# Performance work log

Hardware: AMD Instinct MI355X
Metric: run time of the kernel (lower is better)

## Reference

```python
import jax, jax.numpy as jnp
import numpy as np

H, W = 224, 224
NF, IN_NF, NL = 32, 100, 4


def conv2d(x, w):
    # 3x3 same-padding conv, NCHW / OIHW
    return jax.lax.conv_general_dilated(x, w, (1, 1), [(1, 1), (1, 1)],
                                        dimension_numbers=('NCHW', 'OIHW', 'NCHW'))


def prelu(x, a):
    return jnp.where(x >= 0, x, a[None, :, None, None] * x)


def bilinear_warp(x, flow):
    # backward warp: sample x at (grid + flow), border clamping
    B, C, Hh, Ww = x.shape
    yy, xx = jnp.meshgrid(jnp.arange(Hh, dtype=x.dtype), jnp.arange(Ww, dtype=x.dtype), indexing='ij')
    px = xx[None] + flow[:, 0]  # [B,H,W]
    py = yy[None] + flow[:, 1]
    x0 = jnp.floor(px); y0 = jnp.floor(py)
    wx = (px - x0)[:, None]; wy = (py - y0)[:, None]  # [B,1,H,W]
    cx = lambda v: jnp.clip(v, 0, Ww - 1).astype(jnp.int32)
    cy = lambda v: jnp.clip(v, 0, Hh - 1).astype(jnp.int32)
    x0i, x1i = cx(x0), cx(x0 + 1)
    y0i, y1i = cy(y0), cy(y0 + 1)
    gather = jax.vmap(lambda img, yi, xi: img[:, yi, xi])  # per-batch fancy gather -> [C,H,W]
    I00 = gather(x, y0i, x0i); I01 = gather(x, y0i, x1i)
    I10 = gather(x, y1i, x0i); I11 = gather(x, y1i, x1i)
    return I00 * (1 - wx) * (1 - wy) + I01 * wx * (1 - wy) + I10 * (1 - wx) * wy + I11 * wx * wy


def glblock_forward(feat_0, feat_1, feat_dense, flow, space_mask,
                    w_head, a_head, w_blocks, a_blocks, w_last, b_last, w_mask, b_mask):
    f0w = bilinear_warp(feat_0, flow[:, :2])
    f1w = bilinear_warp(feat_1, flow[:, 2:4])
    x = jnp.concatenate([f0w, f1w, feat_dense, flow], axis=1)  # [1, in_nf, H, W]
    mask_up = jnp.repeat(jnp.repeat(space_mask, 2, axis=2), 2, axis=3)
    # head: conv3x3 (no bias) + PReLU, then spatial masking
    x = prelu(conv2d(x, w_head), a_head) * space_mask
    outs = [x]
    for i in range(w_blocks.shape[0]):
        x = prelu(conv2d(x, w_blocks[i]) * space_mask, a_blocks[i])
        outs.append(x)
    feats = jnp.concatenate(outs, axis=1)  # [1, in_nf*(NL+1), H, W]
    x = jnp.einsum('oi,bihw->bohw', w_last, feats) + b_last[None, :, None, None]  # 1x1 conv
    smn = conv2d(x[:, 4:], w_mask) + b_mask[None, :, None, None]  # [1,2,H,W]
    B, C, Hh, Ww = x.shape
    xu = jax.image.resize(x, (B, C, 2 * Hh, 2 * Ww), 'linear')
    smnu = jax.image.resize(smn, (B, 2, 2 * Hh, 2 * Ww), 'linear')
    flow_out = xu[:, :4]
    feat_t = xu[:, 4:]
    # eval-mode hard routing mask (training uses gumbel-softmax)
    mask_next = (smnu[:, :1] > smnu[:, 1:]).astype(x.dtype) * mask_up
    return flow_out, feat_t, mask_next


def setup_inputs() -> dict:
    key = jax.random.key(0)
    ks = jax.random.split(key, 12)
    r = lambda i, shape, s=1.0: jax.random.normal(ks[i], shape, jnp.float32) * s
    return {
        'feat_0': r(0, (1, NF, H, W)),
        'feat_1': r(1, (1, NF, H, W)),
        'feat_dense': r(2, (1, NF, H, W)),
        'flow': r(3, (1, 4, H, W)),
        'space_mask': jax.random.uniform(ks[4], (1, 1, H, W), jnp.float32),
        'w_head': r(5, (IN_NF, IN_NF, 3, 3), 0.02),
        'a_head': jnp.full((IN_NF,), 0.25, jnp.float32),
        'w_blocks': r(6, (NL, IN_NF, IN_NF, 3, 3), 0.02),
        'a_blocks': jnp.full((NL, IN_NF), 0.25, jnp.float32),
        'w_last': r(7, (4 + NF, IN_NF * (NL + 1)), 0.02),
        'b_last': r(8, (4 + NF,), 0.02),
        'w_mask': r(9, (2, NF, 3, 3), 0.02),
        'b_mask': r(10, (2,), 0.02),
    }


def reference(feat_0, feat_1, feat_dense, flow, space_mask,
              w_head, a_head, w_blocks, a_blocks, w_last, b_last, w_mask, b_mask):
    return glblock_forward(feat_0, feat_1, feat_dense, flow, space_mask,
                           w_head, a_head, w_blocks, a_blocks, w_last, b_last, w_mask, b_mask)
```

## Files before the change

kernel.cpp:

```cpp
#include <hip/hip_runtime.h>
#include <hip/hip_bf16.h>

#define HWs 50176
#define WID 224
#define OHW 200704

typedef __attribute__((ext_vector_type(8))) short s16x8;
typedef __attribute__((ext_vector_type(4))) float f32x4;

static __device__ __forceinline__ unsigned short f2bf(float x) {
  unsigned u = __float_as_uint(x);
  unsigned r = (u + 0x7fffu + ((u >> 16) & 1u)) >> 16;
  return (unsigned short)r;
}
static __device__ __forceinline__ float bf2f(unsigned short b) {
  return __uint_as_float(((unsigned)b) << 16);
}

__global__ void k_wt(const float* __restrict__ w_head, const float* __restrict__ w_blk,
                     unsigned short* __restrict__ bw) {
  int gid = blockIdx.x * 256 + threadIdx.x;
  int frag = gid >> 7, rr = gid & 127;
  int spl = rr >> 6, lane = rr & 63;
  int l = frag / 288, q = frag - l * 288;
  int t = q / 32, q2 = q - t * 32;
  int ck = q2 >> 3, nt = q2 & 7;
  int oc = nt * 16 + (lane & 15);
  int kg = lane >> 4;
  const float* src = (l == 0) ? w_head : (w_blk + (size_t)(l - 1) * 90000);
  s16x8 outv;
  #pragma unroll
  for (int e = 0; e < 8; ++e) {
    int ic = ck * 32 + kg * 8 + e;
    float w = (oc < 100 && ic < 100) ? src[oc * 900 + ic * 9 + t] : 0.f;
    unsigned short h = f2bf(w);
    unsigned short lo = f2bf(w - bf2f(h));
    outv[e] = (short)(spl ? lo : h);
  }
  ((s16x8*)bw)[gid] = outv;
}

__global__ void k_wlT(const float* __restrict__ wlast, float* __restrict__ wlT) {
  int i = blockIdx.x * 256 + threadIdx.x;
  if (i < 18000) {
    int il = i / 36, o = i - il * 36;
    wlT[i] = wlast[o * 500 + il];
  }
}

__global__ void k_binit(const float* __restrict__ blast, float* __restrict__ xlast) {
  int p = blockIdx.x * 256 + threadIdx.x;
  xlast[(size_t)blockIdx.y * HWs + p] = blast[blockIdx.y];
}

__global__ void k_warp(const float* __restrict__ f0, const float* __restrict__ f1,
                       const float* __restrict__ fd, const float* __restrict__ fl,
                       float* __restrict__ xin) {
  int p = blockIdx.x * 256 + threadIdx.x;
  int yq = blockIdx.y;
  int y = p / WID, x = p - y * WID;
  float fx0 = fl[p];
  float fy0 = fl[HWs + p];
  float fx1 = fl[2 * HWs + p];
  float fy1 = fl[3 * HWs + p];

  #pragma unroll
  for (int img = 0; img < 2; ++img) {
    const float* src = img ? f1 : f0;
    float fx = img ? fx1 : fx0;
    float fy = img ? fy1 : fy0;
    float px = (float)x + fx, py = (float)y + fy;
    float x0f = floorf(px), y0f = floorf(py);
    float wx = px - x0f, wy = py - y0f;
    int x0 = (int)fminf(fmaxf(x0f,       0.f), 223.f);
    int x1 = (int)fminf(fmaxf(x0f + 1.f, 0.f), 223.f);
    int y0 = (int)fminf(fmaxf(y0f,       0.f), 223.f);
    int y1 = (int)fminf(fmaxf(y0f + 1.f, 0.f), 223.f);
    float w00 = (1.f - wx) * (1.f - wy), w01 = wx * (1.f - wy);
    float w10 = (1.f - wx) * wy,         w11 = wx * wy;
    int i00 = y0 * WID + x0, i01 = y0 * WID + x1;
    int i10 = y1 * WID + x0, i11 = y1 * WID + x1;
    float* dst = xin + img * 32 * HWs;
    for (int c = yq * 8; c < yq * 8 + 8; ++c) {
      const float* pl = src + c * HWs;
      dst[c * HWs + p] = w00 * pl[i00] + w01 * pl[i01]
                       + w10 * pl[i10] + w11 * pl[i11];
    }
  }
  for (int c = yq * 8; c < yq * 8 + 8; ++c)
    xin[(64 + c) * HWs + p] = fd[c * HWs + p];
  if (yq == 0) {
    xin[96 * HWs + p] = fx0; xin[97 * HWs + p] = fy0;
    xin[98 * HWs + p] = fx1; xin[99 * HWs + p] = fy1;
  }
}

__global__ __launch_bounds__(256) void k_conv(
    const float* __restrict__ in, const unsigned short* __restrict__ bw,
    const float* __restrict__ avec, const float* __restrict__ mask,
    float* __restrict__ out) {
  __shared__ __align__(16) unsigned char sh[2][6 * 34 * 160];
  const int tid = threadIdx.x;
  const int lane = tid & 63;
  const int wv = tid >> 6;
  const int wr = wv >> 1, wz = wv & 1;
  const int c0 = blockIdx.x * 32;
  const int r0 = blockIdx.y * 4;
  const int li = lane & 15, kg = lane >> 4;

  f32x4 acc[4][4];
  #pragma unroll
  for (int a = 0; a < 4; ++a)
    #pragma unroll
    for (int b = 0; b < 4; ++b) acc[a][b] = (f32x4){0.f, 0.f, 0.f, 0.f};

  const s16x8* bp = (const s16x8*)bw;
  s16x8 bcur[4][2], bnxt[4][2];
  #pragma unroll
  for (int nt = 0; nt < 4; ++nt)
    #pragma unroll
    for (int sp = 0; sp < 2; ++sp)
      bnxt[nt][sp] = bp[(((wz * 4 + nt) * 2 + sp) << 6) + lane];

  auto STAGE = [&](int ck, unsigned char* dst) {
    for (int j = tid; j < 816; j += 256) {
      int kgs = j & 3;
      int rc = j >> 2;
      int pr = rc / 34, pc = rc - pr * 34;
      int gy = r0 - 1 + pr, gx = c0 - 1 + pc;
      int gb = ck * 32 + kgs * 8;
      bool inb = ((unsigned)gy < 224u) && ((unsigned)gx < 224u);
      const float* src = in + (size_t)gb * HWs + gy * WID + gx;
      s16x8 hv, lv;
      #pragma unroll
      for (int e = 0; e < 8; ++e) {
        float v = 0.f;
        if (inb && (gb + e) < 100) v = src[(size_t)e * HWs];
        unsigned short h = f2bf(v);
        unsigned short l2 = f2bf(v - bf2f(h));
        hv[e] = (short)h; lv[e] = (short)l2;
      }
      int base = rc * 160, sw = (rc & 7) << 4;
      *(s16x8*)(dst + base + ((kgs * 16) ^ sw)) = hv;
      *(s16x8*)(dst + base + ((64 + kgs * 16) ^ sw)) = lv;
    }
  };

  STAGE(0, sh[0]);
  __syncthreads();

  for (int ck = 0; ck < 4; ++ck) {
    unsigned char* cur = sh[ck & 1];
    if (ck < 3) STAGE(ck + 1, sh[(ck + 1) & 1]);

    #pragma unroll
    for (int t = 0; t < 9; ++t) {
      #pragma unroll
      for (int nt = 0; nt < 4; ++nt) {
        bcur[nt][0] = bnxt[nt][0];
        bcur[nt][1] = bnxt[nt][1];
      }
      if (t < 8 || ck < 3) {
        int nf = (t < 8) ? (t + 1) * 32 + ck * 8 : (ck + 1) * 8;
        #pragma unroll
        for (int nt = 0; nt < 4; ++nt)
          #pragma unroll
          for (int sp = 0; sp < 2; ++sp)
            bnxt[nt][sp] = bp[(((nf + wz * 4 + nt) * 2 + sp) << 6) + lane];
      }
      const int dy = t / 3 - 1, dx = t - (t / 3) * 3 - 1;
      #pragma unroll
      for (int ms = 0; ms < 4; ++ms) {
        int pr = wr * 2 + (ms >> 1) + 1 + dy;
        int pc = (ms & 1) * 16 + li + 1 + dx;
        int rc = pr * 34 + pc;
        int base = rc * 160, sw = (rc & 7) << 4;
        s16x8 ah = *(const s16x8*)(cur + base + ((kg * 16) ^ sw));
        s16x8 al = *(const s16x8*)(cur + base + ((64 + kg * 16) ^ sw));
        #pragma unroll
        for (int nt = 0; nt < 4; ++nt) {
          acc[ms][nt] = __builtin_amdgcn_mfma_f32_16x16x32_bf16(ah, bcur[nt][0], acc[ms][nt], 0, 0, 0);
          acc[ms][nt] = __builtin_amdgcn_mfma_f32_16x16x32_bf16(al, bcur[nt][0], acc[ms][nt], 0, 0, 0);
          acc[ms][nt] = __builtin_amdgcn_mfma_f32_16x16x32_bf16(ah, bcur[nt][1], acc[ms][nt], 0, 0, 0);
        }
      }
    }
    __syncthreads();
  }

  float4 mv[4];
  #pragma unroll
  for (int ms = 0; ms < 4; ++ms) {
    int row = r0 + wr * 2 + (ms >> 1);
    int colb = c0 + (ms & 1) * 16 + kg * 4;
    mv[ms] = *(const float4*)&mask[row * WID + colb];
  }
  #pragma unroll
  for (int nt = 0; nt < 4; ++nt) {
    int oc = wz * 64 + nt * 16 + li;
    if (oc < 100) {
      float a = avec[oc];
      #pragma unroll
      for (int ms = 0; ms < 4; ++ms) {
        int row = r0 + wr * 2 + (ms >> 1);
        int colb = c0 + (ms & 1) * 16 + kg * 4;
        f32x4 zv = acc[ms][nt];
        float4 o;
        o.x = (zv.x >= 0.f ? zv.x : a * zv.x) * mv[ms].x;
        o.y = (zv.y >= 0.f ? zv.y : a * zv.y) * mv[ms].y;
        o.z = (zv.z >= 0.f ? zv.z : a * zv.z) * mv[ms].z;
        o.w = (zv.w >= 0.f ? zv.w : a * zv.w) * mv[ms].w;
        *(float4*)&out[(size_t)oc * HWs + row * WID + colb] = o;
      }
    }
  }
}

__global__ __launch_bounds__(64) void k_esum(
    const float* __restrict__ A0, const float* __restrict__ A1,
    const float* __restrict__ A2, const float* __restrict__ A3,
    const float* __restrict__ A4, const float* __restrict__ wlT,
    float* __restrict__ xlast) {
  int p = blockIdx.x * 64 + threadIdx.x;
  int l = blockIdx.y;
  const float* a = (l == 0) ? A0 : (l == 1) ? A1 : (l == 2) ? A2 : (l == 3) ? A3 : A4;
  const float* w = wlT + l * 3600;
  float acc[36];
  #pragma unroll
  for (int o = 0; o < 36; ++o) acc[o] = 0.f;
  for (int c0 = 0; c0 < 100; c0 += 10) {
    float v[10];
    #pragma unroll
    for (int q = 0; q < 10; ++q)
      v[q] = a[(size_t)(c0 + q) * HWs + p];
    #pragma unroll
    for (int q = 0; q < 10; ++q) {
      const float4* wp = (const float4*)(w + (c0 + q) * 36);
      #pragma unroll
      for (int j = 0; j < 9; ++j) {
        float4 t = wp[j];
        acc[4*j]   = fmaf(t.x, v[q], acc[4*j]);
        acc[4*j+1] = fmaf(t.y, v[q], acc[4*j+1]);
        acc[4*j+2] = fmaf(t.z, v[q], acc[4*j+2]);
        acc[4*j+3] = fmaf(t.w, v[q], acc[4*j+3]);
      }
    }
  }
  #pragma unroll
  for (int o = 0; o < 36; ++o)
    atomicAdd(&xlast[(size_t)o * HWs + p], acc[o]);
}

__global__ void k_smn(const float* __restrict__ xlast, const float* __restrict__ wmask,
                      const float* __restrict__ bmask, float* __restrict__ smnh) {
  __shared__ float wm[288];
  int tid = threadIdx.x;
  int h = blockIdx.y;
  for (int j = tid; j < 288; j += 64) {
    int o = j / 144, r = j - o * 144;
    wm[j] = wmask[o * 288 + h * 144 + r];
  }
  __syncthreads();
  int p = blockIdx.x * 64 + tid;
  int y = p / WID, x = p - y * WID;
  double a0 = 0.0, a1 = 0.0;
  for (int icl = 0; icl < 16; ++icl) {
    const float* pl = xlast + (size_t)(4 + h * 16 + icl) * HWs;
    #pragma unroll
    for (int dy = -1; dy <= 1; ++dy) {
      int gy = y + dy;
      if ((unsigned)gy < 224u) {
        #pragma unroll
        for (int dx = -1; dx <= 1; ++dx) {
          int gx = x + dx;
          if ((unsigned)gx < 224u) {
            double v = (double)pl[gy * WID + gx];
            int t = (dy + 1) * 3 + (dx + 1);
            a0 += (double)wm[icl * 9 + t] * v;
            a1 += (double)wm[144 + icl * 9 + t] * v;
          }
        }
      }
    }
  }
  if (h == 0) { a0 += (double)bmask[0]; a1 += (double)bmask[1]; }
  smnh[(size_t)(h * 2 + 0) * HWs + p] = (float)a0;
  smnh[(size_t)(h * 2 + 1) * HWs + p] = (float)a1;
}

__global__ void k_upsample(const float* __restrict__ xlast, const float* __restrict__ smnh,
                           const float* __restrict__ smask, float* __restrict__ out) {
  int q = blockIdx.x * 256 + threadIdx.x;
  int oy = q / 448, ox = q - oy * 448;
  int ky = oy >> 1, kx = ox >> 1;
  int r0, r1, c0, c1; float wy0, wy1, wx0, wx1;
  if (oy & 1) { r0 = ky; r1 = (ky < 223) ? ky + 1 : 223; wy0 = 0.75f; wy1 = 0.25f; }
  else        { r0 = (ky > 0) ? ky - 1 : 0; r1 = ky;     wy0 = 0.25f; wy1 = 0.75f; }
  if (ox & 1) { c0 = kx; c1 = (kx < 223) ? kx + 1 : 223; wx0 = 0.75f; wx1 = 0.25f; }
  else        { c0 = (kx > 0) ? kx - 1 : 0; c1 = kx;     wx0 = 0.25f; wx1 = 0.75f; }
  float w00 = wy0 * wx0, w01 = wy0 * wx1, w10 = wy1 * wx0, w11 = wy1 * wx1;
  int i00 = r0 * WID + c0, i01 = r0 * WID + c1, i10 = r1 * WID + c0, i11 = r1 * WID + c1;
  for (int ch = 0; ch < 36; ++ch) {
    const float* pl = xlast + (size_t)ch * HWs;
    out[(size_t)ch * OHW + q] = w00 * pl[i00] + w01 * pl[i01]
                              + w10 * pl[i10] + w11 * pl[i11];
  }
  const float* sa0 = smnh;
  const float* sa1 = smnh + HWs;
  const float* sb0 = smnh + 2 * HWs;
  const float* sb1 = smnh + 3 * HWs;
  double s0 = (double)w00 * ((double)sa0[i00] + (double)sb0[i00])
            + (double)w01 * ((double)sa0[i01] + (double)sb0[i01])
            + (double)w10 * ((double)sa0[i10] + (double)sb0[i10])
            + (double)w11 * ((double)sa0[i11] + (double)sb0[i11]);
  double s1 = (double)w00 * ((double)sa1[i00] + (double)sb1[i00])
            + (double)w01 * ((double)sa1[i01] + (double)sb1[i01])
            + (double)w10 * ((double)sa1[i10] + (double)sb1[i10])
            + (double)w11 * ((double)sa1[i11] + (double)sb1[i11]);
  float mu = smask[ky * WID + kx];
  out[36 * OHW + q] = (s0 > s1) ? mu : 0.f;
}

extern "C" void kernel_launch(void* const* d_in, const int* in_sizes, int n_in,
                              void* d_out, int out_size, void* d_ws, size_t ws_size,
                              hipStream_t stream) {
  const float* feat0   = (const float*)d_in[0];
  const float* feat1   = (const float*)d_in[1];
  const float* featd   = (const float*)d_in[2];
  const float* flow    = (const float*)d_in[3];
  const float* smask   = (const float*)d_in[4];
  const float* w_head  = (const float*)d_in[5];
  const float* a_head  = (const float*)d_in[6];
  const float* w_blk   = (const float*)d_in[7];
  const float* a_blk   = (const float*)d_in[8];
  const float* w_last  = (const float*)d_in[9];
  const float* b_last  = (const float*)d_in[10];
  const float* w_mask  = (const float*)d_in[11];
  const float* b_mask  = (const float*)d_in[12];

  float* B0 = (float*)d_ws;
  float* B1 = B0 + (size_t)100 * HWs;
  float* B2 = B1 + (size_t)100 * HWs;
  float* B3 = B2 + (size_t)100 * HWs;
  float* B4 = B3 + (size_t)100 * HWs;
  float* smnh = B4 + (size_t)100 * HWs;
  float* wlT  = smnh + (size_t)4 * HWs;
  float* xlast = wlT + 18000;
  unsigned short* bw = (unsigned short*)xlast;

  k_wt<<<dim3(720), 256, 0, stream>>>(w_head, w_blk, bw);
  k_wlT<<<dim3(71), 256, 0, stream>>>(w_last, wlT);
  k_warp<<<dim3(196, 4), 256, 0, stream>>>(feat0, feat1, featd, flow, B0);

  dim3 cgrid(7, 56);
  k_conv<<<cgrid, 256, 0, stream>>>(B0, bw,               a_head,      smask, B1);
  k_conv<<<cgrid, 256, 0, stream>>>(B1, bw + 1 * 294912,  a_blk,       smask, B0);
  k_conv<<<cgrid, 256, 0, stream>>>(B0, bw + 2 * 294912,  a_blk + 100, smask, B2);
  k_conv<<<cgrid, 256, 0, stream>>>(B2, bw + 3 * 294912,  a_blk + 200, smask, B3);
  k_conv<<<cgrid, 256, 0, stream>>>(B3, bw + 4 * 294912,  a_blk + 300, smask, B4);

  k_binit<<<dim3(196, 36), 256, 0, stream>>>(b_last, xlast);
  k_esum<<<dim3(784, 5), 64, 0, stream>>>(B1, B0, B2, B3, B4, wlT, xlast);

  k_smn<<<dim3(784, 2), 64, 0, stream>>>(xlast, w_mask, b_mask, smnh);
  k_upsample<<<784, 256, 0, stream>>>(xlast, smnh, smask, (float*)d_out);
}
```

Baseline: 462.7 us.

## Split conv K-reduction across two wave groups with LDS reduction

The 3x3 conv kernel now launches 512 threads per block. Each group of 256 threads handles half of the four input-channel chunks, and the two groups' partial accumulators are summed through shared memory before the PReLU/mask epilogue. This doubles the waves available per output tile to hide latency and shortens the serial K loop. In exchange, the old double-buffered staging overlap is dropped in favour of separate stage-then-sync phases, and an LDS reduction plus extra barriers are added. Shared memory grows to 64KB per block, which may limit occupancy.

```diff
diff --git a/kernel.cpp b/kernel.cpp
--- a/kernel.cpp
+++ b/kernel.cpp
@@ -95,18 +95,21 @@
   }
 }
 
-__global__ __launch_bounds__(256) void k_conv(
+__global__ __launch_bounds__(512, 4) void k_conv(
     const float* __restrict__ in, const unsigned short* __restrict__ bw,
     const float* __restrict__ avec, const float* __restrict__ mask,
     float* __restrict__ out) {
-  __shared__ __align__(16) unsigned char sh[2][6 * 34 * 160];
+  __shared__ __align__(16) unsigned char sh[65536];
   const int tid = threadIdx.x;
   const int lane = tid & 63;
-  const int wv = tid >> 6;
-  const int wr = wv >> 1, wz = wv & 1;
+  const int g = tid >> 8;
+  const int gt = tid & 255;
+  const int wq = (tid >> 6) & 3;
+  const int wr = wq >> 1, wz = wq & 1;
   const int c0 = blockIdx.x * 32;
   const int r0 = blockIdx.y * 4;
   const int li = lane & 15, kg = lane >> 4;
+  unsigned char* buf = sh + g * 32640;
 
   f32x4 acc[4][4];
   #pragma unroll
@@ -120,10 +123,10 @@
   for (int nt = 0; nt < 4; ++nt)
     #pragma unroll
     for (int sp = 0; sp < 2; ++sp)
-      bnxt[nt][sp] = bp[(((wz * 4 + nt) * 2 + sp) << 6) + lane];
-
-  auto STAGE = [&](int ck, unsigned char* dst) {
-    for (int j = tid; j < 816; j += 256) {
+      bnxt[nt][sp] = bp[(((16 * g + wz * 4 + nt) * 2 + sp) << 6) + lane];
+
+  auto STAGE = [&](int ck) {
+    for (int j = gt; j < 816; j += 256) {
       int kgs = j & 3;
       int rc = j >> 2;
       int pr = rc / 34, pc = rc - pr * 34;
@@ -141,18 +144,16 @@
         hv[e] = (short)h; lv[e] = (short)l2;
       }
       int base = rc * 160, sw = (rc & 7) << 4;
-      *(s16x8*)(dst + base + ((kgs * 16) ^ sw)) = hv;
-      *(s16x8*)(dst + base + ((64 + kgs * 16) ^ sw)) = lv;
+      *(s16x8*)(buf + base + ((kgs * 16) ^ sw)) = hv;
+      *(s16x8*)(buf + base + ((64 + kgs * 16) ^ sw)) = lv;
     }
   };
 
-  STAGE(0, sh[0]);
+  STAGE(2 * g);
   __syncthreads();
 
-  for (int ck = 0; ck < 4; ++ck) {
-    unsigned char* cur = sh[ck & 1];
-    if (ck < 3) STAGE(ck + 1, sh[(ck + 1) & 1]);
-
+  for (int s = 0; s < 2; ++s) {
+    int ck = 2 * g + s;
     #pragma unroll
     for (int t = 0; t < 9; ++t) {
       #pragma unroll
@@ -160,8 +161,8 @@
         bcur[nt][0] = bnxt[nt][0];
         bcur[nt][1] = bnxt[nt][1];
       }
-      if (t < 8 || ck < 3) {
-        int nf = (t < 8) ? (t + 1) * 32 + ck * 8 : (ck + 1) * 8;
+      if (t < 8 || s == 0) {
+        int nf = (t < 8) ? (t + 1) * 32 + ck * 8 : (2 * g + 1) * 8;
         #pragma unroll
         for (int nt = 0; nt < 4; ++nt)
           #pragma unroll
@@ -175,8 +176,8 @@
         int pc = (ms & 1) * 16 + li + 1 + dx;
         int rc = pr * 34 + pc;
         int base = rc * 160, sw = (rc & 7) << 4;
-        s16x8 ah = *(const s16x8*)(cur + base + ((kg * 16) ^ sw));
-        s16x8 al = *(const s16x8*)(cur + base + ((64 + kg * 16) ^ sw));
+        s16x8 ah = *(const s16x8*)(buf + base + ((kg * 16) ^ sw));
+        s16x8 al = *(const s16x8*)(buf + base + ((64 + kg * 16) ^ sw));
         #pragma unroll
         for (int nt = 0; nt < 4; ++nt) {
           acc[ms][nt] = __builtin_amdgcn_mfma_f32_16x16x32_bf16(ah, bcur[nt][0], acc[ms][nt], 0, 0, 0);
@@ -186,31 +187,55 @@
       }
     }
     __syncthreads();
-  }
-
-  float4 mv[4];
-  #pragma unroll
-  for (int ms = 0; ms < 4; ++ms) {
-    int row = r0 + wr * 2 + (ms >> 1);
-    int colb = c0 + (ms & 1) * 16 + kg * 4;
-    mv[ms] = *(const float4*)&mask[row * WID + colb];
-  }
-  #pragma unroll
-  for (int nt = 0; nt < 4; ++nt) {
-    int oc = wz * 64 + nt * 16 + li;
-    if (oc < 100) {
-      float a = avec[oc];
-      #pragma unroll
-      for (int ms = 0; ms < 4; ++ms) {
-        int row = r0 + wr * 2 + (ms >> 1);
-        int colb = c0 + (ms & 1) * 16 + kg * 4;
-        f32x4 zv = acc[ms][nt];
-        float4 o;
-        o.x = (zv.x >= 0.f ? zv.x : a * zv.x) * mv[ms].x;
-        o.y = (zv.y >= 0.f ? zv.y : a * zv.y) * mv[ms].y;
-        o.z = (zv.z >= 0.f ? zv.z : a * zv.z) * mv[ms].z;
-        o.w = (zv.w >= 0.f ? zv.w : a * zv.w) * mv[ms].w;
-        *(float4*)&out[(size_t)oc * HWs + row * WID + colb] = o;
+    if (s == 0) {
+      STAGE(2 * g + 1);
+      __syncthreads();
+    }
+  }
+
+  float* red = (float*)sh;
+  if (g == 1) {
+    #pragma unroll
+    for (int ms = 0; ms < 4; ++ms)
+      #pragma unroll
+      for (int nt = 0; nt < 4; ++nt)
+        *(f32x4*)&red[(size_t)(wq * 16 + ms * 4 + nt) * 256 + lane * 4] = acc[ms][nt];
+  }
+  __syncthreads();
+  if (g == 0) {
+    #pragma unroll
+    for (int ms = 0; ms < 4; ++ms)
+      #pragma unroll
+      for (int nt = 0; nt < 4; ++nt) {
+        f32x4 o = *(const f32x4*)&red[(size_t)(wq * 16 + ms * 4 + nt) * 256 + lane * 4];
+        acc[ms][nt].x += o.x; acc[ms][nt].y += o.y;
+        acc[ms][nt].z += o.z; acc[ms][nt].w += o.w;
+      }
+
+    float4 mv[4];
+    #pragma unroll
+    for (int ms = 0; ms < 4; ++ms) {
+      int row = r0 + wr * 2 + (ms >> 1);
+      int colb = c0 + (ms & 1) * 16 + kg * 4;
+      mv[ms] = *(const float4*)&mask[row * WID + colb];
+    }
+    #pragma unroll
+    for (int nt = 0; nt < 4; ++nt) {
+      int oc = wz * 64 + nt * 16 + li;
+      if (oc < 100) {
+        float a = avec[oc];
+        #pragma unroll
+        for (int ms = 0; ms < 4; ++ms) {
+          int row = r0 + wr * 2 + (ms >> 1);
+          int colb = c0 + (ms & 1) * 16 + kg * 4;
+          f32x4 zv = acc[ms][nt];
+          float4 o;
+          o.x = (zv.x >= 0.f ? zv.x : a * zv.x) * mv[ms].x;
+          o.y = (zv.y >= 0.f ? zv.y : a * zv.y) * mv[ms].y;
+          o.z = (zv.z >= 0.f ? zv.z : a * zv.z) * mv[ms].z;
+          o.w = (zv.w >= 0.f ? zv.w : a * zv.w) * mv[ms].w;
+          *(float4*)&out[(size_t)oc * HWs + row * WID + colb] = o;
+        }
       }
     }
   }
@@ -353,11 +378,11 @@
   k_warp<<<dim3(196, 4), 256, 0, stream>>>(feat0, feat1, featd, flow, B0);
 
   dim3 cgrid(7, 56);
-  k_conv<<<cgrid, 256, 0, stream>>>(B0, bw,               a_head,      smask, B1);
-  k_conv<<<cgrid, 256, 0, stream>>>(B1, bw + 1 * 294912,  a_blk,       smask, B0);
-  k_conv<<<cgrid, 256, 0, stream>>>(B0, bw + 2 * 294912,  a_blk + 100, smask, B2);
-  k_conv<<<cgrid, 256, 0, stream>>>(B2, bw + 3 * 294912,  a_blk + 200, smask, B3);
-  k_conv<<<cgrid, 256, 0, stream>>>(B3, bw + 4 * 294912,  a_blk + 300, smask, B4);
+  k_conv<<<cgrid, 512, 0, stream>>>(B0, bw,               a_head,      smask, B1);
+  k_conv<<<cgrid, 512, 0, stream>>>(B1, bw + 1 * 294912,  a_blk,       smask, B0);
+  k_conv<<<cgrid, 512, 0, stream>>>(B0, bw + 2 * 294912,  a_blk + 100, smask, B2);
+  k_conv<<<cgrid, 512, 0, stream>>>(B2, bw + 3 * 294912,  a_blk + 200, smask, B3);
+  k_conv<<<cgrid, 512, 0, stream>>>(B3, bw + 4 * 294912,  a_blk + 300, smask, B4);
 
   k_binit<<<dim3(196, 36), 256, 0, stream>>>(b_last, xlast);
   k_esum<<<dim3(784, 5), 64, 0, stream>>>(B1, B0, B2, B3, B4, wlT, xlast);
```

Measured after the change: 989.1 us. 2.14x slower.

## Split conv tile to two rows with four waves each covering 32 output channels

Applied to the files above, without the earlier changes.

The conv block tile drops from 4 output rows to 2, and the four waves now split the 128 padded output channels four ways instead of a 2x2 row/channel split. The grid doubles to 784 blocks, and per-wave accumulators and weight registers halve, which should raise occupancy and give more blocks per CU. In exchange the halo overhead grows (4 staged rows for 2 output rows instead of 6 for 4), so input staging and bf16 hi/lo conversion per output rises, and each wave re-reads the same A fragments for fewer MFMAs.

```diff
diff --git a/kernel.cpp b/kernel.cpp
--- a/kernel.cpp
+++ b/kernel.cpp
@@ -99,31 +99,30 @@
     const float* __restrict__ in, const unsigned short* __restrict__ bw,
     const float* __restrict__ avec, const float* __restrict__ mask,
     float* __restrict__ out) {
-  __shared__ __align__(16) unsigned char sh[2][6 * 34 * 160];
+  __shared__ __align__(16) unsigned char sh[2][4 * 34 * 160];
   const int tid = threadIdx.x;
   const int lane = tid & 63;
-  const int wv = tid >> 6;
-  const int wr = wv >> 1, wz = wv & 1;
+  const int wq = tid >> 6;
   const int c0 = blockIdx.x * 32;
-  const int r0 = blockIdx.y * 4;
+  const int r0 = blockIdx.y * 2;
   const int li = lane & 15, kg = lane >> 4;
 
-  f32x4 acc[4][4];
+  f32x4 acc[4][2];
   #pragma unroll
   for (int a = 0; a < 4; ++a)
     #pragma unroll
-    for (int b = 0; b < 4; ++b) acc[a][b] = (f32x4){0.f, 0.f, 0.f, 0.f};
+    for (int b = 0; b < 2; ++b) acc[a][b] = (f32x4){0.f, 0.f, 0.f, 0.f};
 
   const s16x8* bp = (const s16x8*)bw;
-  s16x8 bcur[4][2], bnxt[4][2];
-  #pragma unroll
-  for (int nt = 0; nt < 4; ++nt)
+  s16x8 bcur[2][2], bnxt[2][2];
+  #pragma unroll
+  for (int ntl = 0; ntl < 2; ++ntl)
     #pragma unroll
     for (int sp = 0; sp < 2; ++sp)
-      bnxt[nt][sp] = bp[(((wz * 4 + nt) * 2 + sp) << 6) + lane];
+      bnxt[ntl][sp] = bp[(((wq * 2 + ntl) * 2 + sp) << 6) + lane];
 
   auto STAGE = [&](int ck, unsigned char* dst) {
-    for (int j = tid; j < 816; j += 256) {
+    for (int j = tid; j < 544; j += 256) {
       int kgs = j & 3;
       int rc = j >> 2;
       int pr = rc / 34, pc = rc - pr * 34;
@@ -156,32 +155,32 @@
     #pragma unroll
     for (int t = 0; t < 9; ++t) {
       #pragma unroll
-      for (int nt = 0; nt < 4; ++nt) {
-        bcur[nt][0] = bnxt[nt][0];
-        bcur[nt][1] = bnxt[nt][1];
+      for (int ntl = 0; ntl < 2; ++ntl) {
+        bcur[ntl][0] = bnxt[ntl][0];
+        bcur[ntl][1] = bnxt[ntl][1];
       }
       if (t < 8 || ck < 3) {
         int nf = (t < 8) ? (t + 1) * 32 + ck * 8 : (ck + 1) * 8;
         #pragma unroll
-        for (int nt = 0; nt < 4; ++nt)
+        for (int ntl = 0; ntl < 2; ++ntl)
           #pragma unroll
           for (int sp = 0; sp < 2; ++sp)
-            bnxt[nt][sp] = bp[(((nf + wz * 4 + nt) * 2 + sp) << 6) + lane];
+            bnxt[ntl][sp] = bp[(((nf + wq * 2 + ntl) * 2 + sp) << 6) + lane];
       }
       const int dy = t / 3 - 1, dx = t - (t / 3) * 3 - 1;
       #pragma unroll
       for (int ms = 0; ms < 4; ++ms) {
-        int pr = wr * 2 + (ms >> 1) + 1 + dy;
+        int pr = (ms >> 1) + 1 + dy;
         int pc = (ms & 1) * 16 + li + 1 + dx;
         int rc = pr * 34 + pc;
         int base = rc * 160, sw = (rc & 7) << 4;
         s16x8 ah = *(const s16x8*)(cur + base + ((kg * 16) ^ sw));
         s16x8 al = *(const s16x8*)(cur + base + ((64 + kg * 16) ^ sw));
         #pragma unroll
-        for (int nt = 0; nt < 4; ++nt) {
-          acc[ms][nt] = __builtin_amdgcn_mfma_f32_16x16x32_bf16(ah, bcur[nt][0], acc[ms][nt], 0, 0, 0);
-          acc[ms][nt] = __builtin_amdgcn_mfma_f32_16x16x32_bf16(al, bcur[nt][0], acc[ms][nt], 0, 0, 0);
-          acc[ms][nt] = __builtin_amdgcn_mfma_f32_16x16x32_bf16(ah, bcur[nt][1], acc[ms][nt], 0, 0, 0);
+        for (int ntl = 0; ntl < 2; ++ntl) {
+          acc[ms][ntl] = __builtin_amdgcn_mfma_f32_16x16x32_bf16(ah, bcur[ntl][0], acc[ms][ntl], 0, 0, 0);
+          acc[ms][ntl] = __builtin_amdgcn_mfma_f32_16x16x32_bf16(al, bcur[ntl][0], acc[ms][ntl], 0, 0, 0);
+          acc[ms][ntl] = __builtin_amdgcn_mfma_f32_16x16x32_bf16(ah, bcur[ntl][1], acc[ms][ntl], 0, 0, 0);
         }
       }
     }
@@ -191,20 +190,20 @@
   float4 mv[4];
   #pragma unroll
   for (int ms = 0; ms < 4; ++ms) {
-    int row = r0 + wr * 2 + (ms >> 1);
+    int row = r0 + (ms >> 1);
     int colb = c0 + (ms & 1) * 16 + kg * 4;
     mv[ms] = *(const float4*)&mask[row * WID + colb];
   }
   #pragma unroll
-  for (int nt = 0; nt < 4; ++nt) {
-    int oc = wz * 64 + nt * 16 + li;
+  for (int ntl = 0; ntl < 2; ++ntl) {
+    int oc = wq * 32 + ntl * 16 + li;
     if (oc < 100) {
       float a = avec[oc];
       #pragma unroll
       for (int ms = 0; ms < 4; ++ms) {
-        int row = r0 + wr * 2 + (ms >> 1);
+        int row = r0 + (ms >> 1);
         int colb = c0 + (ms & 1) * 16 + kg * 4;
-        f32x4 zv = acc[ms][nt];
+        f32x4 zv = acc[ms][ntl];
         float4 o;
         o.x = (zv.x >= 0.f ? zv.x : a * zv.x) * mv[ms].x;
         o.y = (zv.y >= 0.f ? zv.y : a * zv.y) * mv[ms].y;
@@ -352,7 +351,7 @@
   k_wlT<<<dim3(71), 256, 0, stream>>>(w_last, wlT);
   k_warp<<<dim3(196, 4), 256, 0, stream>>>(feat0, feat1, featd, flow, B0);
 
-  dim3 cgrid(7, 56);
+  dim3 cgrid(7, 112);
   k_conv<<<cgrid, 256, 0, stream>>>(B0, bw,               a_head,      smask, B1);
   k_conv<<<cgrid, 256, 0, stream>>>(B1, bw + 1 * 294912,  a_blk,       smask, B0);
   k_conv<<<cgrid, 256, 0, stream>>>(B0, bw + 2 * 294912,  a_blk + 100, smask, B2);
```

New measurement: 534.3 us. 15.5% more time.

## Switch intermediate activations from channel-planar to pixel-major (HWC) layout

Applied to the files above, without the earlier changes.

The warp kernel now writes the 100-channel input pixel-major, the conv kernel stages its input from that layout with float4 loads and writes its output pixel-major, and the 1x1 reduction kernel reads contiguous per-pixel channel vectors. The goal is to replace eight strided per-channel loads in conv staging with two vector loads, and to vectorize the esum reads. In exchange the conv epilogue now does scalar stores strided by 100 floats across lanes, which coalesces poorly, and the warp kernel's per-pixel float4 stores are strided as well.

```diff
diff --git a/kernel.cpp b/kernel.cpp
--- a/kernel.cpp
+++ b/kernel.cpp
@@ -63,6 +63,7 @@
   float fy0 = fl[HWs + p];
   float fx1 = fl[2 * HWs + p];
   float fy1 = fl[3 * HWs + p];
+  float* dst = xin + (size_t)p * 100;
 
   #pragma unroll
   for (int img = 0; img < 2; ++img) {
@@ -80,19 +81,27 @@
     float w10 = (1.f - wx) * wy,         w11 = wx * wy;
     int i00 = y0 * WID + x0, i01 = y0 * WID + x1;
     int i10 = y1 * WID + x0, i11 = y1 * WID + x1;
-    float* dst = xin + img * 32 * HWs;
-    for (int c = yq * 8; c < yq * 8 + 8; ++c) {
-      const float* pl = src + c * HWs;
-      dst[c * HWs + p] = w00 * pl[i00] + w01 * pl[i01]
-                       + w10 * pl[i10] + w11 * pl[i11];
-    }
-  }
-  for (int c = yq * 8; c < yq * 8 + 8; ++c)
-    xin[(64 + c) * HWs + p] = fd[c * HWs + p];
-  if (yq == 0) {
-    xin[96 * HWs + p] = fx0; xin[97 * HWs + p] = fy0;
-    xin[98 * HWs + p] = fx1; xin[99 * HWs + p] = fy1;
-  }
+    float ov[8];
+    #pragma unroll
+    for (int e = 0; e < 8; ++e) {
+      const float* pl = src + (size_t)(yq * 8 + e) * HWs;
+      ov[e] = w00 * pl[i00] + w01 * pl[i01] + w10 * pl[i10] + w11 * pl[i11];
+    }
+    float* d = dst + img * 32 + yq * 8;
+    *(float4*)(d)     = make_float4(ov[0], ov[1], ov[2], ov[3]);
+    *(float4*)(d + 4) = make_float4(ov[4], ov[5], ov[6], ov[7]);
+  }
+  {
+    float ov[8];
+    #pragma unroll
+    for (int e = 0; e < 8; ++e)
+      ov[e] = fd[(size_t)(yq * 8 + e) * HWs + p];
+    float* d = dst + 64 + yq * 8;
+    *(float4*)(d)     = make_float4(ov[0], ov[1], ov[2], ov[3]);
+    *(float4*)(d + 4) = make_float4(ov[4], ov[5], ov[6], ov[7]);
+  }
+  if (yq == 0)
+    *(float4*)(dst + 96) = make_float4(fx0, fy0, fx1, fy1);
 }
 
 __global__ __launch_bounds__(256) void k_conv(
@@ -129,16 +138,21 @@
       int pr = rc / 34, pc = rc - pr * 34;
       int gy = r0 - 1 + pr, gx = c0 - 1 + pc;
       int gb = ck * 32 + kgs * 8;
-      bool inb = ((unsigned)gy < 224u) && ((unsigned)gx < 224u);
-      const float* src = in + (size_t)gb * HWs + gy * WID + gx;
+      bool inb = ((unsigned)gy < 224u) && ((unsigned)gx < 224u) && (gb < 100);
+      float4 va = make_float4(0.f, 0.f, 0.f, 0.f);
+      float4 vb = make_float4(0.f, 0.f, 0.f, 0.f);
+      if (inb) {
+        const float* src = in + (size_t)(gy * WID + gx) * 100 + gb;
+        va = *(const float4*)src;
+        if (gb < 96) vb = *(const float4*)(src + 4);
+      }
+      float vs[8] = {va.x, va.y, va.z, va.w, vb.x, vb.y, vb.z, vb.w};
       s16x8 hv, lv;
       #pragma unroll
       for (int e = 0; e < 8; ++e) {
-        float v = 0.f;
-        if (inb && (gb + e) < 100) v = src[(size_t)e * HWs];
-        unsigned short h = f2bf(v);
-        unsigned short l2 = f2bf(v - bf2f(h));
-        hv[e] = (short)h; lv[e] = (short)l2;
+        unsigned short h = f2bf(vs[e]);
+        hv[e] = (short)h;
+        lv[e] = (short)f2bf(vs[e] - bf2f(h));
       }
       int base = rc * 160, sw = (rc & 7) << 4;
       *(s16x8*)(dst + base + ((kgs * 16) ^ sw)) = hv;
@@ -205,12 +219,13 @@
         int row = r0 + wr * 2 + (ms >> 1);
         int colb = c0 + (ms & 1) * 16 + kg * 4;
         f32x4 zv = acc[ms][nt];
-        float4 o;
-        o.x = (zv.x >= 0.f ? zv.x : a * zv.x) * mv[ms].x;
-        o.y = (zv.y >= 0.f ? zv.y : a * zv.y) * mv[ms].y;
-        o.z = (zv.z >= 0.f ? zv.z : a * zv.z) * mv[ms].z;
-        o.w = (zv.w >= 0.f ? zv.w : a * zv.w) * mv[ms].w;
-        *(float4*)&out[(size_t)oc * HWs + row * WID + colb] = o;
+        float vv[4] = {zv.x, zv.y, zv.z, zv.w};
+        float mm[4] = {mv[ms].x, mv[ms].y, mv[ms].z, mv[ms].w};
+        #pragma unroll
+        for (int e = 0; e < 4; ++e) {
+          float v = (vv[e] >= 0.f ? vv[e] : a * vv[e]) * mm[e];
+          out[(size_t)(row * WID + colb + e) * 100 + oc] = v;
+        }
       }
     }
   }
@@ -223,26 +238,32 @@
     float* __restrict__ xlast) {
   int p = blockIdx.x * 64 + threadIdx.x;
   int l = blockIdx.y;
-  const float* a = (l == 0) ? A0 : (l == 1) ? A1 : (l == 2) ? A2 : (l == 3) ? A3 : A4;
+  const float* ab = (l == 0) ? A0 : (l == 1) ? A1 : (l == 2) ? A2 : (l == 3) ? A3 : A4;
+  const float* a = ab + (size_t)p * 100;
   const float* w = wlT + l * 3600;
   float acc[36];
   #pragma unroll
   for (int o = 0; o < 36; ++o) acc[o] = 0.f;
-  for (int c0 = 0; c0 < 100; c0 += 10) {
-    float v[10];
-    #pragma unroll
-    for (int q = 0; q < 10; ++q)
-      v[q] = a[(size_t)(c0 + q) * HWs + p];
-    #pragma unroll
-    for (int q = 0; q < 10; ++q) {
-      const float4* wp = (const float4*)(w + (c0 + q) * 36);
-      #pragma unroll
-      for (int j = 0; j < 9; ++j) {
-        float4 t = wp[j];
-        acc[4*j]   = fmaf(t.x, v[q], acc[4*j]);
-        acc[4*j+1] = fmaf(t.y, v[q], acc[4*j+1]);
-        acc[4*j+2] = fmaf(t.z, v[q], acc[4*j+2]);
-        acc[4*j+3] = fmaf(t.w, v[q], acc[4*j+3]);
+  for (int cb = 0; cb < 100; cb += 20) {
+    float4 v4[5];
+    #pragma unroll
+    for (int q = 0; q < 5; ++q)
+      v4[q] = *(const float4*)(a + cb + q * 4);
+    #pragma unroll
+    for (int q = 0; q < 5; ++q) {
+      float ve[4] = {v4[q].x, v4[q].y, v4[q].z, v4[q].w};
+      #pragma unroll
+      for (int e = 0; e < 4; ++e) {
+        float v = ve[e];
+        const float4* wp = (const float4*)(w + (cb + q * 4 + e) * 36);
+        #pragma unroll
+        for (int j = 0; j < 9; ++j) {
+          float4 t = wp[j];
+          acc[4*j]   = fmaf(t.x, v, acc[4*j]);
+          acc[4*j+1] = fmaf(t.y, v, acc[4*j+1]);
+          acc[4*j+2] = fmaf(t.z, v, acc[4*j+2]);
+          acc[4*j+3] = fmaf(t.w, v, acc[4*j+3]);
+        }
       }
     }
   }
```

After: 577.1 us. 1.25x slower.
